# Performance work log

Measured on AMD Instinct MI355X. Metric: run time of the kernel, lower is better.

Reference implementation:

```python
import jax, jax.numpy as jnp
import numpy as np
from jax import lax

START = 0  # label_dict['<START>']
END = 8    # label_dict['<END>']
NEG = -10000.0


def setup_inputs() -> dict:
    key = jax.random.key(0)
    k1, k2, k3 = jax.random.split(key, 3)
    B, S, C = 8192, 512, 9
    emission = jax.random.normal(k1, (B, S, C), dtype=jnp.float32)
    # transition_matrix ~ normal, then START row / END column masked to -10000
    T = jax.random.normal(k2, (C, C), dtype=jnp.float32)
    T = T.at[START, :].set(NEG).at[:, END].set(NEG)
    labels = jax.random.randint(k3, (B, S), 0, 8, dtype=jnp.int32)
    mask = jnp.ones((B, S), dtype=jnp.int32)
    return {"emission": emission, "transition": T, "labels": labels, "mask": mask}


def _log_partition(emission, T, mask_f):
    # emission: [B,S,C], T: [C,C], mask_f: [B,S] float
    B, S, C = emission.shape
    init = jnp.full((B, C), NEG, dtype=emission.dtype).at[:, 0].set(0.0)

    def step(log_alpha, inp):
        em_t, m_t = inp  # [B,C], [B,1]
        # add[b,i,j] = log_alpha[b,i] + em_t[b,j] + T[i,j]
        add = log_alpha[:, :, None] + em_t[:, None, :] + T[None, :, :]
        new = jax.nn.logsumexp(add, axis=1)  # [B,C]
        log_alpha = new * m_t + log_alpha * (1.0 - m_t)
        return log_alpha, None

    em_sw = jnp.swapaxes(emission, 0, 1)          # [S,B,C]
    m_sw = jnp.swapaxes(mask_f, 0, 1)[:, :, None]  # [S,B,1]
    final, _ = lax.scan(step, init, (em_sw, m_sw))
    final = final + T[:, END][None, :]
    return jax.nn.logsumexp(final, axis=1)  # [B]


def _sentence_score(emission, T, labels, mask_f):
    B, S, C = emission.shape
    # prepend <START>=0 label
    labels_ext = jnp.concatenate(
        [jnp.full((B, 1), START, dtype=labels.dtype), labels], axis=1)  # [B,S+1]
    # emission score at the gold label of each position
    emit = jnp.take_along_axis(emission, labels[:, :, None].astype(jnp.int32), axis=2)[..., 0]  # [B,S]
    trans = T[labels_ext[:, :-1], labels_ext[:, 1:]]  # [B,S]
    scores = jnp.sum((emit + trans) * mask_f, axis=1)  # [B]
    lengths = jnp.sum(mask_f, axis=1).astype(jnp.int32)  # [B]
    last_label = labels_ext[jnp.arange(B), lengths]       # label at position len in ext seq
    scores = scores + T[last_label, END]
    return scores


def reference(emission, transition, labels, mask):
    mask_f = mask.astype(emission.dtype)
    log_Z = _log_partition(emission, transition, mask_f)
    gold = _sentence_score(emission, transition, labels, mask_f)
    loss = jnp.mean(log_Z - gold)
    return loss
```

## Files before the change

### kernel.cpp

```cpp
#include <hip/hip_runtime.h>


#define CC 9
#define SS 512
#define NEGV (-10000.0f)
#define BLOCKT 256
#define BPW 8
#define BPB 32

template <int M>
__device__ __forceinline__ float rotf(float v) {
    return __int_as_float(__builtin_amdgcn_update_dpp(
        0, __float_as_int(v), 0x120 + 2 * M, 0xF, 0xF, false));
}
template <int M>
__device__ __forceinline__ int roti(int v) {
    return __builtin_amdgcn_update_dpp(0, v, 0x120 + 2 * M, 0xF, 0xF, false);
}

struct Chunk {
    float em[8];
    int lab[8];
    int msk[8];
};

struct St {
    float q, offset, goldtr, goldem;
    int len, prev;
};

__device__ __forceinline__ void load_chunk(Chunk& c, const float* emp,
                                           const int* labp, const int* mskp, int t0) {
#pragma unroll
    for (int k = 0; k < 8; ++k) c.em[k] = emp[(t0 + k) * CC];
    int4 l0 = *(const int4*)(labp + t0);
    int4 l1 = *(const int4*)(labp + t0 + 4);
    int4 m0 = *(const int4*)(mskp + t0);
    int4 m1 = *(const int4*)(mskp + t0 + 4);
    c.lab[0] = l0.x; c.lab[1] = l0.y; c.lab[2] = l0.z; c.lab[3] = l0.w;
    c.lab[4] = l1.x; c.lab[5] = l1.y; c.lab[6] = l1.z; c.lab[7] = l1.w;
    c.msk[0] = m0.x; c.msk[1] = m0.y; c.msk[2] = m0.z; c.msk[3] = m0.w;
    c.msk[4] = m1.x; c.msk[5] = m1.y; c.msk[6] = m1.z; c.msk[7] = m1.w;
}

template <bool RENORM>
__device__ __forceinline__ void crf_step(St& st, float e, float em, int lab, int msk,
                                         float tv, const float* w, int o) {
    float q = st.q;
    float g1 = rotf<1>(q), g2 = rotf<2>(q), g3 = rotf<3>(q);
    float g4 = rotf<4>(q), g5 = rotf<5>(q), g6 = rotf<6>(q), g7 = rotf<7>(q);
    float s0 = q * w[0];
    float s1 = g1 * w[1];
    float s2 = g2 * w[2];
    s0 = fmaf(g3, w[3], s0);
    s1 = fmaf(g4, w[4], s1);
    s2 = fmaf(g5, w[5], s2);
    s0 = fmaf(g6, w[6], s0);
    s1 = fmaf(g7, w[7], s1);
    float ssum = s0 + (s1 + s2);
    bool m = (msk != 0);
    st.goldtr += m ? tv : 0.0f;
    st.goldem += (m && lab == o) ? em : 0.0f;
    st.len += m ? 1 : 0;
    float nq = m ? ssum * e : q;
    if (RENORM) {
        float mx = fmaxf(nq, rotf<1>(nq));
        mx = fmaxf(mx, rotf<2>(mx));
        mx = fmaxf(mx, rotf<4>(mx));
        nq *= __builtin_amdgcn_rcpf(mx);
        st.offset += __logf(mx);
    }
    st.q = nq;
}

__device__ __forceinline__ void consume8(St& st, const Chunk& c, const float* Tl,
                                         const float* w, int o) {
    float tv[8];
    tv[0] = Tl[st.prev * CC + c.lab[0]];
#pragma unroll
    for (int k = 1; k < 8; ++k) tv[k] = Tl[c.lab[k - 1] * CC + c.lab[k]];
    st.prev = c.lab[7];
    float e[8];
#pragma unroll
    for (int k = 0; k < 8; ++k) e[k] = __expf(c.em[k]);
    crf_step<true >(st, e[0], c.em[0], c.lab[0], c.msk[0], tv[0], w, o);
    crf_step<false>(st, e[1], c.em[1], c.lab[1], c.msk[1], tv[1], w, o);
    crf_step<false>(st, e[2], c.em[2], c.lab[2], c.msk[2], tv[2], w, o);
    crf_step<false>(st, e[3], c.em[3], c.lab[3], c.msk[3], tv[3], w, o);
    crf_step<true >(st, e[4], c.em[4], c.lab[4], c.msk[4], tv[4], w, o);
    crf_step<false>(st, e[5], c.em[5], c.lab[5], c.msk[5], tv[5], w, o);
    crf_step<false>(st, e[6], c.em[6], c.lab[6], c.msk[6], tv[6], w, o);
    crf_step<false>(st, e[7], c.em[7], c.lab[7], c.msk[7], tv[7], w, o);
}

__global__ __launch_bounds__(BLOCKT, 1) void crf_main(
    const float* __restrict__ emission, const float* __restrict__ transition,
    const int* __restrict__ labels, const int* __restrict__ mask,
    float* __restrict__ out, int B, float invB) {
    __shared__ float Tl[CC * CC];
    __shared__ float blocksum;
    int tid = threadIdx.x;
    if (tid == 0) blocksum = 0.0f;
    for (int i = tid; i < CC * CC; i += BLOCKT) Tl[i] = transition[i];
    __syncthreads();

    int lane = tid & 63, wv = tid >> 6;
    int pos = lane & 15, row = lane >> 4;
    int par = pos & 1, s = pos >> 1;
    int o = s;
    long batch = (long)blockIdx.x * BPB + wv * BPW + row * 2 + par;
    bool valid = batch < (long)B;
    size_t bidx = valid ? (size_t)batch : 0;

    int ssrc[8];
    ssrc[0] = s;
    ssrc[1] = roti<1>(s); ssrc[2] = roti<2>(s); ssrc[3] = roti<3>(s);
    ssrc[4] = roti<4>(s); ssrc[5] = roti<5>(s); ssrc[6] = roti<6>(s);
    ssrc[7] = roti<7>(s);
    float wmain[8], wf[8];
#pragma unroll
    for (int m = 0; m < 8; ++m) {
        int is_ = ssrc[m];
        wmain[m] = __expf(Tl[is_ * CC + o]);
        wf[m] = __expf(Tl[(is_ == 0 ? 8 : is_) * CC + o]);
    }

    float mT8 = Tl[8];
#pragma unroll
    for (int i = 1; i < CC; ++i) mT8 = fmaxf(mT8, Tl[i * CC + 8]);
    float wend = __expf(Tl[o * CC + 8] - mT8);

    int colq = (s == 0) ? 8 : s;
    float v, vref;
    {
        float mx1 = Tl[colq], mx2 = Tl[1];
#pragma unroll
        for (int i = 1; i < CC; ++i) {
            mx1 = fmaxf(mx1, NEGV + Tl[i * CC + colq]);
            mx2 = fmaxf(mx2, NEGV + Tl[i * CC + 1]);
        }
        float a1 = __expf(Tl[colq] - mx1), a2 = __expf(Tl[1] - mx2);
#pragma unroll
        for (int i = 1; i < CC; ++i) {
            a1 += __expf(NEGV + Tl[i * CC + colq] - mx1);
            a2 += __expf(NEGV + Tl[i * CC + 1] - mx2);
        }
        v = mx1 + __logf(a1);
        vref = mx2 + __logf(a2);
    }

    const float* emp = emission + bidx * (SS * CC) + o;
    const int* labp = labels + bidx * SS;
    const int* mskp = mask + bidx * SS;
    float em8 = emission[bidx * (SS * CC) + 8];

    Chunk A, Bc;
    load_chunk(A, emp, labp, mskp, 0);
    load_chunk(Bc, emp, labp, mskp, 8);

    St st;
    st.q = 0.f; st.offset = 0.f; st.goldtr = 0.f; st.goldem = 0.f;
    st.len = 0; st.prev = 0;

    {
        bool m0 = (A.msk[0] != 0);
        float em0q = (s == 0) ? em8 : A.em[0];
        st.q = m0 ? __expf(v + em0q - vref) : 0.0f;
        st.offset = m0 ? vref : 0.0f;
        st.goldtr = m0 ? Tl[A.lab[0]] : 0.0f;
        st.goldem = (m0 && A.lab[0] == o) ? A.em[0] : 0.0f;
        st.len = m0 ? 1 : 0;
    }
    {
        float tv[8];
#pragma unroll
        for (int k = 1; k < 8; ++k) tv[k] = Tl[A.lab[k - 1] * CC + A.lab[k]];
        st.prev = A.lab[7];
        float e[8];
#pragma unroll
        for (int k = 1; k < 8; ++k) e[k] = __expf(A.em[k]);
        crf_step<false>(st, e[1], A.em[1], A.lab[1], A.msk[1], tv[1], wf, o);
        crf_step<false>(st, e[2], A.em[2], A.lab[2], A.msk[2], tv[2], wmain, o);
        crf_step<false>(st, e[3], A.em[3], A.lab[3], A.msk[3], tv[3], wmain, o);
        crf_step<true >(st, e[4], A.em[4], A.lab[4], A.msk[4], tv[4], wmain, o);
        crf_step<false>(st, e[5], A.em[5], A.lab[5], A.msk[5], tv[5], wmain, o);
        crf_step<false>(st, e[6], A.em[6], A.lab[6], A.msk[6], tv[6], wmain, o);
        crf_step<false>(st, e[7], A.em[7], A.lab[7], A.msk[7], tv[7], wmain, o);
    }
    load_chunk(A, emp, labp, mskp, 16);

    for (int c = 1; c <= 61; c += 2) {
        consume8(st, Bc, Tl, wmain, o);
        load_chunk(Bc, emp, labp, mskp, (c + 2) * 8);
        consume8(st, A, Tl, wmain, o);
        if (c + 3 <= 63) load_chunk(A, emp, labp, mskp, (c + 3) * 8);
    }
    consume8(st, Bc, Tl, wmain, o);

    int lastlab = (st.len > 0) ? labp[st.len - 1] : 0;
    float gend = Tl[lastlab * CC + 8];
    float fin = st.q * wend;
    float sw = fin + rotf<1>(fin);
    sw = sw + rotf<2>(sw);
    sw = sw + rotf<4>(sw);
    float gpart = st.goldem + ((s == 0) ? (st.goldtr + gend) : 0.0f);
    float sg = gpart + rotf<1>(gpart);
    sg = sg + rotf<2>(sg);
    sg = sg + rotf<4>(sg);
    if (valid && s == 0) {
        float logZ = st.offset + mT8 + __logf(sw);
        atomicAdd(&blocksum, (logZ - sg) * invB);
    }
    __syncthreads();
    if (tid == 0) atomicAdd(out, blocksum);
}

extern "C" void kernel_launch(void* const* d_in, const int* in_sizes, int n_in,
                              void* d_out, int out_size, void* d_ws, size_t ws_size,
                              hipStream_t stream) {
    const float* emission = (const float*)d_in[0];
    const float* transition = (const float*)d_in[1];
    const int* labels = (const int*)d_in[2];
    const int* mask = (const int*)d_in[3];
    float* out = (float*)d_out;

    int B = in_sizes[2] / SS;
    float invB = 1.0f / (float)B;

    hipMemsetAsync(out, 0, sizeof(float) * out_size, stream);
    int nblocks = (B + BPB - 1) / BPB;
    crf_main<<<nblocks, BLOCKT, 0, stream>>>(emission, transition, labels, mask,
                                             out, B, invB);
}
```

Baseline: 249.3 us.

## Deepen chunk prefetch and decouple renormalization from the serial recurrence

```diff
diff --git a/kernel.cpp b/kernel.cpp
--- a/kernel.cpp
+++ b/kernel.cpp
@@ -18,16 +18,10 @@
     return __builtin_amdgcn_update_dpp(0, v, 0x120 + 2 * M, 0xF, 0xF, false);
 }
 
-struct Chunk {
-    float em[8];
-    int lab[8];
-    int msk[8];
-};
-
-struct St {
-    float q, offset, goldtr, goldem;
-    int len, prev;
-};
+struct Chunk { float em[8]; int lab[8]; int msk[8]; };
+struct Aux   { float a[8];  float mf[8]; float tvv[8]; };
+struct St    { float q, offset, goldtr, goldem, lenf; };
+struct Rn    { float r, nlg; };
 
 __device__ __forceinline__ void load_chunk(Chunk& c, const float* emp,
                                            const int* labp, const int* mskp, int t0) {
@@ -43,54 +37,85 @@
     c.msk[4] = m1.x; c.msk[5] = m1.y; c.msk[6] = m1.z; c.msk[7] = m1.w;
 }
 
-template <bool RENORM>
-__device__ __forceinline__ void crf_step(St& st, float e, float em, int lab, int msk,
-                                         float tv, const float* w, int o) {
+__device__ __forceinline__ void make_aux(Aux& X, const Chunk& c, int prevlab,
+                                         St& st, const float* Tl, int o) {
+    int pl = prevlab;
+#pragma unroll
+    for (int k = 0; k < 8; ++k) {
+        float mf = (float)c.msk[k];
+        float e = __expf(c.em[k]);
+        X.mf[k] = mf;
+        X.a[k] = e * mf;
+        X.tvv[k] = Tl[pl * CC + c.lab[k]];
+        pl = c.lab[k];
+        float gsel = (c.lab[k] == o) ? c.em[k] : 0.0f;
+        st.goldem = fmaf(gsel, mf, st.goldem);
+        st.lenf += mf;
+    }
+}
+
+__device__ __forceinline__ Rn kick(float q) {
+    float t = fmaxf(q, rotf<1>(q));
+    t = fmaxf(t, rotf<2>(t));
+    t = fmaxf(t, rotf<4>(t));
+    t = fmaxf(t, 1e-35f);
+    Rn rn;
+    rn.r = __builtin_amdgcn_rcpf(t);
+    rn.nlg = -__logf(rn.r);
+    return rn;
+}
+
+template <bool KICK, bool FOLD>
+__device__ __forceinline__ void stepk(St& st, const Aux& X, int k,
+                                      const float* w, Rn& rn) {
     float q = st.q;
+    if (KICK) rn = kick(q);
     float g1 = rotf<1>(q), g2 = rotf<2>(q), g3 = rotf<3>(q);
     float g4 = rotf<4>(q), g5 = rotf<5>(q), g6 = rotf<6>(q), g7 = rotf<7>(q);
-    float s0 = q * w[0];
-    float s1 = g1 * w[1];
-    float s2 = g2 * w[2];
+    float s0 = q * w[0], s1 = g1 * w[1], s2 = g2 * w[2];
     s0 = fmaf(g3, w[3], s0);
     s1 = fmaf(g4, w[4], s1);
     s2 = fmaf(g5, w[5], s2);
     s0 = fmaf(g6, w[6], s0);
     s1 = fmaf(g7, w[7], s1);
-    float ssum = s0 + (s1 + s2);
-    bool m = (msk != 0);
-    st.goldtr += m ? tv : 0.0f;
-    st.goldem += (m && lab == o) ? em : 0.0f;
-    st.len += m ? 1 : 0;
-    float nq = m ? ssum * e : q;
-    if (RENORM) {
-        float mx = fmaxf(nq, rotf<1>(nq));
-        mx = fmaxf(mx, rotf<2>(mx));
-        mx = fmaxf(mx, rotf<4>(mx));
-        nq *= __builtin_amdgcn_rcpf(mx);
-        st.offset += __logf(mx);
-    }
-    st.q = nq;
-}
-
-__device__ __forceinline__ void consume8(St& st, const Chunk& c, const float* Tl,
-                                         const float* w, int o) {
-    float tv[8];
-    tv[0] = Tl[st.prev * CC + c.lab[0]];
-#pragma unroll
-    for (int k = 1; k < 8; ++k) tv[k] = Tl[c.lab[k - 1] * CC + c.lab[k]];
-    st.prev = c.lab[7];
-    float e[8];
-#pragma unroll
-    for (int k = 0; k < 8; ++k) e[k] = __expf(c.em[k]);
-    crf_step<true >(st, e[0], c.em[0], c.lab[0], c.msk[0], tv[0], w, o);
-    crf_step<false>(st, e[1], c.em[1], c.lab[1], c.msk[1], tv[1], w, o);
-    crf_step<false>(st, e[2], c.em[2], c.lab[2], c.msk[2], tv[2], w, o);
-    crf_step<false>(st, e[3], c.em[3], c.lab[3], c.msk[3], tv[3], w, o);
-    crf_step<true >(st, e[4], c.em[4], c.lab[4], c.msk[4], tv[4], w, o);
-    crf_step<false>(st, e[5], c.em[5], c.lab[5], c.msk[5], tv[5], w, o);
-    crf_step<false>(st, e[6], c.em[6], c.lab[6], c.msk[6], tv[6], w, o);
-    crf_step<false>(st, e[7], c.em[7], c.lab[7], c.msk[7], tv[7], w, o);
+    float s = s0 + (s1 + s2);
+    float ak = X.a[k];
+    float pb = fmaf(-X.mf[k], q, q);
+    if (FOLD) { ak *= rn.r; pb *= rn.r; st.offset += rn.nlg; }
+    st.q = fmaf(s, ak, pb);
+}
+
+__device__ __forceinline__ void consume(St& st, const Aux& X, const float* w) {
+    Rn rn;
+    stepk<true , false>(st, X, 0, w, rn);
+    stepk<false, true >(st, X, 1, w, rn);
+    stepk<false, false>(st, X, 2, w, rn);
+    stepk<false, false>(st, X, 3, w, rn);
+    stepk<true , false>(st, X, 4, w, rn);
+    stepk<false, true >(st, X, 5, w, rn);
+    stepk<false, false>(st, X, 6, w, rn);
+    stepk<false, false>(st, X, 7, w, rn);
+#pragma unroll
+    for (int k = 0; k < 8; ++k) st.goldtr = fmaf(X.tvv[k], X.mf[k], st.goldtr);
+}
+
+__device__ __forceinline__ void consume0(St& st, const Chunk& c, const Aux& X,
+                                         const float* wmain, const float* wf,
+                                         float v, float vref, float em8, int s_slot) {
+    bool m0 = (c.msk[0] != 0);
+    float em0q = (s_slot == 0) ? em8 : c.em[0];
+    st.q = m0 ? __expf(v + em0q - vref) : 0.0f;
+    st.offset = m0 ? vref : 0.0f;
+    Rn rn = kick(st.q);
+    stepk<false, true >(st, X, 1, wf, rn);
+    stepk<false, false>(st, X, 2, wmain, rn);
+    stepk<false, false>(st, X, 3, wmain, rn);
+    stepk<true , false>(st, X, 4, wmain, rn);
+    stepk<false, true >(st, X, 5, wmain, rn);
+    stepk<false, false>(st, X, 6, wmain, rn);
+    stepk<false, false>(st, X, 7, wmain, rn);
+#pragma unroll
+    for (int k = 0; k < 8; ++k) st.goldtr = fmaf(X.tvv[k], X.mf[k], st.goldtr);
 }
 
 __global__ __launch_bounds__(BLOCKT, 1) void crf_main(
@@ -104,11 +129,11 @@
     for (int i = tid; i < CC * CC; i += BLOCKT) Tl[i] = transition[i];
     __syncthreads();
 
-    int lane = tid & 63, wv = tid >> 6;
+    int lane = tid & 63;
     int pos = lane & 15, row = lane >> 4;
     int par = pos & 1, s = pos >> 1;
     int o = s;
-    long batch = (long)blockIdx.x * BPB + wv * BPW + row * 2 + par;
+    long batch = (long)blockIdx.x * BPB + (tid >> 6) * BPW + row * 2 + par;
     bool valid = batch < (long)B;
     size_t bidx = valid ? (size_t)batch : 0;
 
@@ -154,50 +179,43 @@
     const int* mskp = mask + bidx * SS;
     float em8 = emission[bidx * (SS * CC) + 8];
 
-    Chunk A, Bc;
-    load_chunk(A, emp, labp, mskp, 0);
-    load_chunk(Bc, emp, labp, mskp, 8);
-
-    St st;
-    st.q = 0.f; st.offset = 0.f; st.goldtr = 0.f; st.goldem = 0.f;
-    st.len = 0; st.prev = 0;
-
-    {
-        bool m0 = (A.msk[0] != 0);
-        float em0q = (s == 0) ? em8 : A.em[0];
-        st.q = m0 ? __expf(v + em0q - vref) : 0.0f;
-        st.offset = m0 ? vref : 0.0f;
-        st.goldtr = m0 ? Tl[A.lab[0]] : 0.0f;
-        st.goldem = (m0 && A.lab[0] == o) ? A.em[0] : 0.0f;
-        st.len = m0 ? 1 : 0;
-    }
-    {
-        float tv[8];
-#pragma unroll
-        for (int k = 1; k < 8; ++k) tv[k] = Tl[A.lab[k - 1] * CC + A.lab[k]];
-        st.prev = A.lab[7];
-        float e[8];
-#pragma unroll
-        for (int k = 1; k < 8; ++k) e[k] = __expf(A.em[k]);
-        crf_step<false>(st, e[1], A.em[1], A.lab[1], A.msk[1], tv[1], wf, o);
-        crf_step<false>(st, e[2], A.em[2], A.lab[2], A.msk[2], tv[2], wmain, o);
-        crf_step<false>(st, e[3], A.em[3], A.lab[3], A.msk[3], tv[3], wmain, o);
-        crf_step<true >(st, e[4], A.em[4], A.lab[4], A.msk[4], tv[4], wmain, o);
-        crf_step<false>(st, e[5], A.em[5], A.lab[5], A.msk[5], tv[5], wmain, o);
-        crf_step<false>(st, e[6], A.em[6], A.lab[6], A.msk[6], tv[6], wmain, o);
-        crf_step<false>(st, e[7], A.em[7], A.lab[7], A.msk[7], tv[7], wmain, o);
-    }
-    load_chunk(A, emp, labp, mskp, 16);
-
-    for (int c = 1; c <= 61; c += 2) {
-        consume8(st, Bc, Tl, wmain, o);
-        load_chunk(Bc, emp, labp, mskp, (c + 2) * 8);
-        consume8(st, A, Tl, wmain, o);
-        if (c + 3 <= 63) load_chunk(A, emp, labp, mskp, (c + 3) * 8);
-    }
-    consume8(st, Bc, Tl, wmain, o);
-
-    int lastlab = (st.len > 0) ? labp[st.len - 1] : 0;
+    Chunk b0, b1, b2, b3;
+    load_chunk(b0, emp, labp, mskp, 0 * 8);
+    load_chunk(b1, emp, labp, mskp, 1 * 8);
+    load_chunk(b2, emp, labp, mskp, 2 * 8);
+    load_chunk(b3, emp, labp, mskp, 3 * 8);
+
+    St st; st.q = 0.f; st.offset = 0.f; st.goldtr = 0.f; st.goldem = 0.f; st.lenf = 0.f;
+    Aux X, Y;
+
+    make_aux(X, b0, 0, st, Tl, o);
+    consume0(st, b0, X, wmain, wf, v, vref, em8, s);
+    int p = b0.lab[7];
+    make_aux(X, b1, p, st, Tl, o);
+    load_chunk(b0, emp, labp, mskp, 4 * 8);
+
+    for (int c = 1; c <= 57; c += 4) {
+        make_aux(Y, b2, b1.lab[7], st, Tl, o);
+        consume(st, X, wmain);
+        load_chunk(b1, emp, labp, mskp, (c + 4 > 63 ? 63 : c + 4) * 8);
+        make_aux(X, b3, b2.lab[7], st, Tl, o);
+        consume(st, Y, wmain);
+        load_chunk(b2, emp, labp, mskp, (c + 5 > 63 ? 63 : c + 5) * 8);
+        make_aux(Y, b0, b3.lab[7], st, Tl, o);
+        consume(st, X, wmain);
+        load_chunk(b3, emp, labp, mskp, (c + 6 > 63 ? 63 : c + 6) * 8);
+        make_aux(X, b1, b0.lab[7], st, Tl, o);
+        consume(st, Y, wmain);
+        load_chunk(b0, emp, labp, mskp, (c + 7 > 63 ? 63 : c + 7) * 8);
+    }
+    make_aux(Y, b2, b1.lab[7], st, Tl, o);
+    consume(st, X, wmain);
+    make_aux(X, b3, b2.lab[7], st, Tl, o);
+    consume(st, Y, wmain);
+    consume(st, X, wmain);
+
+    int len = (int)(st.lenf + 0.5f);
+    int lastlab = (len > 0) ? labp[len - 1] : 0;
     float gend = Tl[lastlab * CC + 8];
     float fin = st.q * wend;
     float sw = fin + rotf<1>(fin);
```

New measurement: 259.3 us. 4.0% more time.
